# Optimization experiments

Measured on AMD Instinct MI355X. Metric: run time of the kernel, lower is better.

Reference implementation:

```python
import jax, jax.numpy as jnp
import numpy as np

B, U1, U2 = 4, 2048, 2048
C = 256      # in_feat_dim
F = 256      # feat_dim
M = 4        # num_modes
D = C // M   # attention_mode_dim = 64
ATTN_CLIP = 500.0
LN_EPS = 1e-12


def setup_inputs() -> dict:
    key = jax.random.key(0)
    ks = jax.random.split(key, 8)
    s = 0.02  # base_initializer_range
    inp = {
        "query_feat": jax.random.normal(ks[0], (B, U1, C), jnp.float32),
        "key_feat": jax.random.normal(ks[1], (B, U2, C), jnp.float32),
        "Wq": jax.random.normal(ks[2], (M * D, C), jnp.float32) * s,
        "bq": jnp.zeros((M * D,), jnp.float32),
    }
    # tie_qk_scheme='shared': key linear shares query weights
    inp["Wk"] = inp["Wq"]
    inp["bk"] = inp["bq"]
    inp["Wv"] = jax.random.normal(ks[3], (M * F, C), jnp.float32) * s  # first_linear, v_has_bias=False
    inp["W_mid"] = jax.random.normal(ks[4], (F, F), jnp.float32) * s   # MMSharedMid shared_linear
    inp["b_mid"] = jnp.zeros((F,), jnp.float32)
    inp["W_out"] = jax.random.normal(ks[5], (M, F, F), jnp.float32) * s  # grouped 1x1 conv, per mode
    inp["b_out"] = jnp.zeros((M, F), jnp.float32)
    inp["ln_g"] = jnp.ones((F,), jnp.float32)   # resout LayerNorm
    inp["ln_b"] = jnp.zeros((F,), jnp.float32)
    inp["W_score"] = jax.random.normal(ks[6], (1, F), jnp.float32) * s  # LearnedSoftAggregate
    inp["b_score"] = jnp.zeros((1,), jnp.float32)
    return inp


def _layer_norm(x, g, b):
    mu = jnp.mean(x, axis=-1, keepdims=True)
    var = jnp.var(x, axis=-1, keepdims=True)
    return (x - mu) * jax.lax.rsqrt(var + LN_EPS) * g + b


def reference(query_feat, key_feat, Wq, bq, Wk, bk, Wv, W_mid, b_mid,
              W_out, b_out, ln_g, ln_b, W_score, b_score):
    # --- tied-QK multi-mode attention ---
    q = (query_feat @ Wq.T + bq).reshape(B, U1, M, D)
    k = (key_feat @ Wk.T + bk).reshape(B, U2, M, D)
    scores = jnp.einsum('bimd,bjmd->bmij', q, k) / jnp.sqrt(jnp.float32(D))
    scores = jnp.clip(scores, -ATTN_CLIP, ATTN_CLIP)  # attn_clip
    probs = jax.nn.softmax(scores, axis=-1)           # [B, M, U1, U2]

    # --- ExpandedFeatTrans: value projection + fusion ---
    v = (key_feat @ Wv.T).reshape(B, U2, M, F)        # first_linear (no bias)
    fused = jnp.einsum('bmij,bjmf->bmif', probs, v)   # [B, M, U1, F]

    # MMSharedMid: shared linear over F + gelu (dropout = identity in eval)
    mid = jax.nn.gelu(fused @ W_mid.T + b_mid, approximate=False)

    # MMPrivateOutput: per-mode grouped 1x1 conv; NOTE the original code computes
    # x_comb = x + shortcut but then layer-norms x (shortcut dropped) - kept faithful.
    out = jnp.einsum('bmif,mgf->bmig', mid, W_out) + b_out[None, :, None, :]
    out = _layer_norm(out, ln_g, ln_b)                # [B, M, U1, F]

    # LearnedSoftAggregate over modes (group_dim=1, keepdim=False)
    mode_scores = out @ W_score.T + b_score           # [B, M, U1, 1]
    mode_probs = jax.nn.softmax(mode_scores, axis=1)
    return jnp.sum(out * mode_probs, axis=1)          # [B, U1, F]
```

## Files before the change

kernel.cpp:

```cpp
#include <hip/hip_runtime.h>

typedef __attribute__((ext_vector_type(8))) short short8;
typedef __attribute__((ext_vector_type(4))) float f32x4;
typedef __attribute__((ext_vector_type(16))) float f32x16;
typedef unsigned short u16t;
typedef unsigned int u32t;

#define MFMA16(a, b, c) __builtin_amdgcn_mfma_f32_16x16x32_bf16((a), (b), (c), 0, 0, 0)
#define MFMA32(a, b, c) __builtin_amdgcn_mfma_f32_32x32x16_bf16((a), (b), (c), 0, 0, 0)

__device__ __forceinline__ u16t f2bf(float f) {
  u32t u = __float_as_uint(f);
  u32t r = u + 0x7fffu + ((u >> 16) & 1u);
  return (u16t)(r >> 16);
}
__device__ __forceinline__ float bf2f(u16t b) {
  return __uint_as_float(((u32t)b) << 16);
}
__device__ __forceinline__ short8 pack8(float4 a0, float4 a1) {
  short8 r;
  r[0] = (short)f2bf(a0.x); r[1] = (short)f2bf(a0.y);
  r[2] = (short)f2bf(a0.z); r[3] = (short)f2bf(a0.w);
  r[4] = (short)f2bf(a1.x); r[5] = (short)f2bf(a1.y);
  r[6] = (short)f2bf(a1.z); r[7] = (short)f2bf(a1.w);
  return r;
}
__device__ __forceinline__ u32t packrhu(float a, float b) {
  u32t ua = __float_as_uint(a) + 0x8000u;
  u32t ub = __float_as_uint(b) + 0x8000u;
  return (ua >> 16) | (ub & 0xffff0000u);
}

__global__ __launch_bounds__(256) void prep_kernel(
    const float* __restrict__ query, const float* __restrict__ key,
    const float* __restrict__ Wq, const float* __restrict__ bq,
    const float* __restrict__ Wv, const float* __restrict__ Wm,
    const float* __restrict__ Wo,
    u16t* __restrict__ WmB, u16t* __restrict__ WoB,
    u16t* __restrict__ QfB, u16t* __restrict__ KfB, u16t* __restrict__ VfB) {
  const int blk = blockIdx.x;
  const int tid = threadIdx.x;

  if (blk >= 768) {
    int cv = blk - 768;
    const float* src; u16t* dst; int base;
    if (cv < 64) { src = Wm; dst = WmB; base = cv * 1024; }
    else         { src = Wo; dst = WoB; base = (cv - 64) * 1024; }
    int i = base + tid * 4;
    float4 v = *(const float4*)(src + i);
    ushort4 o2;
    o2.x = f2bf(v.x); o2.y = f2bf(v.y); o2.z = f2bf(v.z); o2.w = f2bf(v.w);
    *(ushort4*)(dst + i) = o2;
    return;
  }

  __shared__ __align__(16) u16t As[64 * 264];
  __shared__ __align__(16) u16t Ws[64 * 72];

  const int w = tid >> 6, lane = tid & 63, quad = lane >> 4, l15 = lane & 15;
  const int l31 = lane & 31, h8 = (lane >> 5) * 8;
  const int wrow = (w >> 1) * 32, wcol = (w & 1) * 32;
  const int r2 = tid >> 3, c8 = tid & 7;

  const float* A; const float* W; const float* bias;
  float scale; u16t* outp; int mode, bx, by0;
  if (blk < 128) {
    A = query; W = Wq; bias = bq; scale = 0.125f; outp = QfB; mode = 0; bx = blk; by0 = 0;
  } else if (blk < 256) {
    A = key; W = Wq; bias = bq; scale = 1.0f; outp = KfB; mode = 0; bx = blk - 128; by0 = 0;
  } else {
    int v2 = blk - 256;
    A = key; W = Wv; bias = nullptr; scale = 1.0f; outp = VfB; mode = 1;
    bx = v2 & 127; by0 = (v2 >> 7) * 4;
  }
  const int rt = bx * 64;

#pragma unroll
  for (int hh = 0; hh < 2; ++hh) {
    int rr = r2 + hh * 32;
    const float* arow = A + (size_t)(rt + rr) * 256;
#pragma unroll
    for (int kt = 0; kt < 4; ++kt) {
      const float4* pa = (const float4*)(arow + kt * 64 + c8 * 8);
      float4 a0 = pa[0], a1 = pa[1];
      a0.x *= scale; a0.y *= scale; a0.z *= scale; a0.w *= scale;
      a1.x *= scale; a1.y *= scale; a1.z *= scale; a1.w *= scale;
      *(short8*)&As[rr * 264 + kt * 64 + c8 * 8] = pack8(a0, a1);
    }
  }
  __syncthreads();

  short8 af[8][2];
#pragma unroll
  for (int ks8 = 0; ks8 < 8; ++ks8) {
    af[ks8][0] = *(const short8*)&As[(wrow + l15) * 264 + ks8 * 32 + quad * 8];
    af[ks8][1] = *(const short8*)&As[(wrow + 16 + l15) * 264 + ks8 * 32 + quad * 8];
  }

#pragma unroll 1
  for (int nt = 0; nt < 4; ++nt) {
    const int by = by0 + nt;
    const int ct = by * 64;

    const f32x4 fz = {0.f, 0.f, 0.f, 0.f};
    f32x4 acc[2][2];
#pragma unroll
    for (int i = 0; i < 2; i++)
#pragma unroll
      for (int j = 0; j < 2; j++) acc[i][j] = fz;

#pragma unroll
    for (int kt = 0; kt < 4; ++kt) {
      __syncthreads();
#pragma unroll
      for (int hh = 0; hh < 2; ++hh) {
        int rr = r2 + hh * 32;
        const float4* pw = (const float4*)(W + (size_t)(ct + rr) * 256 + kt * 64 + c8 * 8);
        *(short8*)&Ws[rr * 72 + c8 * 8] = pack8(pw[0], pw[1]);
      }
      __syncthreads();
#pragma unroll
      for (int ks = 0; ks < 2; ++ks) {
        short8 bw0 = *(const short8*)&Ws[(wcol + l15) * 72 + ks * 32 + quad * 8];
        short8 bw1 = *(const short8*)&Ws[(wcol + 16 + l15) * 72 + ks * 32 + quad * 8];
        acc[0][0] = MFMA16(af[kt * 2 + ks][0], bw0, acc[0][0]);
        acc[0][1] = MFMA16(af[kt * 2 + ks][0], bw1, acc[0][1]);
        acc[1][0] = MFMA16(af[kt * 2 + ks][1], bw0, acc[1][0]);
        acc[1][1] = MFMA16(af[kt * 2 + ks][1], bw1, acc[1][1]);
      }
    }

    __syncthreads();
    u16t* Cs = Ws;
    if (mode == 0) {
#pragma unroll
      for (int i = 0; i < 2; i++) {
        int rl = wrow + i * 16 + quad * 4;
#pragma unroll
        for (int j = 0; j < 2; j++) {
          int cl = wcol + j * 16 + l15;
          float bv = bias ? bias[ct + cl] * scale : 0.f;
#pragma unroll
          for (int rg = 0; rg < 4; ++rg)
            Cs[(rl + rg) * 72 + cl] = f2bf(acc[i][j][rg] + bv);
        }
      }
    } else {
#pragma unroll
      for (int i = 0; i < 2; i++) {
        int rl = wrow + i * 16 + quad * 4;
#pragma unroll
        for (int j = 0; j < 2; j++) {
          int cl = wcol + j * 16 + l15;
          ushort4 pk;
          pk.x = f2bf(acc[i][j][0]);
          pk.y = f2bf(acc[i][j][1]);
          pk.z = f2bf(acc[i][j][2]);
          pk.w = f2bf(acc[i][j][3]);
          *(ushort4*)&Cs[cl * 72 + rl] = pk;
        }
      }
    }
    __syncthreads();
#pragma unroll
    for (int t2 = 0; t2 < 2; ++t2) {
      short8 frag = *(const short8*)&Cs[(t2 * 32 + l31) * 72 + w * 16 + h8];
      size_t base;
      if (mode == 0) {
        int b = rt >> 11, m = by;
        int it32 = ((rt & 2047) >> 5) + t2;
        base = (((size_t)(b * 4 + m) * 64 + it32) * 4 + w) * 512;
      } else {
        int b = rt >> 11, m = by >> 2;
        int fb = ((by & 3) << 1) + t2;
        int jt16 = ((rt & 2047) >> 4) + w;
        base = (((size_t)(b * 4 + m) * 8 + fb) * 128 + jt16) * 512;
      }
      *(short8*)(outp + base + lane * 8) = frag;
    }
  }
}

__global__ __launch_bounds__(256, 4) void attn_kernel(
    const u16t* __restrict__ Qf, const u16t* __restrict__ Kf,
    const u16t* __restrict__ Vf,
    const u16t* __restrict__ Wmid, const u16t* __restrict__ Wout,
    const float* __restrict__ b_mid, const float* __restrict__ b_out,
    const float* __restrict__ ln_g, const float* __restrict__ ln_b,
    const float* __restrict__ Wsc, const float* __restrict__ b_sc,
    u16t* __restrict__ out_ln, float* __restrict__ scoresWS) {
  __shared__ __align__(16) u16t smU[8448];
  __shared__ float smL[128];
  __shared__ float smR[128];
  __shared__ float smS[64];
  const int tid = threadIdx.x;
  const int w = tid >> 6, lane = tid & 63, quad = lane >> 4, l15 = lane & 15;
  const int l31 = lane & 31, h = lane >> 5;
  const int L = blockIdx.x;
  const int xcd = L & 7, slot = L >> 3;
  const int bm = xcd * 2 + (slot >> 6);
  const int it32 = slot & 63;
  const int m = bm & 3;
  const int q0 = it32 * 32;

  const size_t lane8 = (size_t)lane * 8;

  const u16t* qbase = Qf + ((size_t)(bm * 64 + it32) * 4) * 512 + lane8;
  short8 qf4[4];
#pragma unroll
  for (int ksd = 0; ksd < 4; ++ksd)
    qf4[ksd] = *(const short8*)(qbase + ksd * 512);

  const u16t* kbase = Kf + ((size_t)bm * 256) * 512 + lane8;
  const u16t* vbase = Vf + ((size_t)(bm * 8 + 2 * w) * 128) * 512 + lane8;

  f32x16 facc[2];
#pragma unroll
  for (int j = 0; j < 2; j++)
#pragma unroll
    for (int r = 0; r < 16; r++) facc[j][r] = 0.f;
  float lsum = 0.f;

  short8 kf4[4];
#pragma unroll
  for (int ksd = 0; ksd < 4; ++ksd)
    kf4[ksd] = *(const short8*)(kbase + (size_t)w * 2048 + ksd * 512);

  {
    f32x16 sacc;
#pragma unroll
    for (int r = 0; r < 16; r++) sacc[r] = 0.f;
#pragma unroll
    for (int ksd = 0; ksd < 4; ++ksd)
      sacc = MFMA32(kf4[ksd], qf4[ksd], sacc);
    float ls = 0.f;
#pragma unroll
    for (int tt = 0; tt < 8; ++tt) {
      const int jl = ((2 * tt) & 3) + 8 * ((2 * tt) >> 2) + 4 * h;
      float p0 = __expf(sacc[2 * tt]);
      float p1 = __expf(sacc[2 * tt + 1]);
      ls += p0 + p1;
      *(u32t*)&smU[l31 * 132 + w * 32 + jl] = packrhu(p0, p1);
    }
    lsum += ls;
  }
#pragma unroll
  for (int ksd = 0; ksd < 4; ++ksd)
    kf4[ksd] = *(const short8*)(kbase + (size_t)(4 + w) * 2048 + ksd * 512);
  __syncthreads();

#pragma unroll 1
  for (int t = 0; t < 16; ++t) {
    u16t* Pb = (t & 1) ? smU + 4224 : smU;
    u16t* Pn = (t & 1) ? smU : smU + 4224;

    if (t < 15) {
      f32x16 sacc;
#pragma unroll
      for (int r = 0; r < 16; r++) sacc[r] = 0.f;
#pragma unroll
      for (int ksd = 0; ksd < 4; ++ksd)
        sacc = MFMA32(kf4[ksd], qf4[ksd], sacc);
      float ls = 0.f;
#pragma unroll
      for (int tt = 0; tt < 8; ++tt) {
        const int jl = ((2 * tt) & 3) + 8 * ((2 * tt) >> 2) + 4 * h;
        float p0 = __expf(sacc[2 * tt]);
        float p1 = __expf(sacc[2 * tt + 1]);
        ls += p0 + p1;
        *(u32t*)&Pn[l31 * 132 + w * 32 + jl] = packrhu(p0, p1);
      }
      lsum += ls;
    }
    if (t < 14) {
      const int jn = (t + 2) * 4 + w;
#pragma unroll
      for (int ksd = 0; ksd < 4; ++ksd)
        kf4[ksd] = *(const short8*)(kbase + (size_t)jn * 2048 + ksd * 512);
    }
#pragma unroll
    for (int jj = 0; jj < 4; ++jj) {
      short8 vf[2][2];
#pragma unroll
      for (int fb = 0; fb < 2; ++fb)
#pragma unroll
        for (int ks2 = 0; ks2 < 2; ++ks2)
          vf[fb][ks2] = *(const short8*)(vbase + ((size_t)fb * 128 + (t * 8 + jj * 2 + ks2)) * 512);
      short8 bbL[2];
#pragma unroll
      for (int ks2 = 0; ks2 < 2; ++ks2)
        bbL[ks2] = *(const short8*)&Pb[l31 * 132 + jj * 32 + ks2 * 16 + h * 8];
      facc[0] = MFMA32(vf[0][0], bbL[0], facc[0]);
      facc[0] = MFMA32(vf[0][1], bbL[1], facc[0]);
      facc[1] = MFMA32(vf[1][0], bbL[0], facc[1]);
      facc[1] = MFMA32(vf[1][1], bbL[1], facc[1]);
    }
    __syncthreads();
  }

  lsum += __shfl_xor(lsum, 32);
  if (h == 0) smL[w * 32 + l31] = lsum;
  __syncthreads();
  float inv = 1.f / (smL[l31] + smL[32 + l31] + smL[64 + l31] + smL[96 + l31]);

  u16t* const smF = smU;
#pragma unroll
  for (int fb = 0; fb < 2; ++fb) {
#pragma unroll
    for (int g = 0; g < 4; ++g) {
      int fbase = w * 64 + fb * 32 + 8 * g + 4 * h;
      ushort4 pk4;
      pk4.x = f2bf(facc[fb][4 * g + 0] * inv);
      pk4.y = f2bf(facc[fb][4 * g + 1] * inv);
      pk4.z = f2bf(facc[fb][4 * g + 2] * inv);
      pk4.w = f2bf(facc[fb][4 * g + 3] * inv);
      *(ushort4*)&smF[l31 * 264 + fbase] = pk4;
    }
  }
  __syncthreads();

  const int rgrp = w >> 1, ch = w & 1;
  const int rowq = rgrp * 16 + quad * 4;
  const f32x4 fz4 = {0.f, 0.f, 0.f, 0.f};

  f32x4 macc[8];
#pragma unroll
  for (int i = 0; i < 8; i++) macc[i] = fz4;
  for (int kc = 0; kc < 8; ++kc) {
    short8 af = *(const short8*)&smF[(rgrp * 16 + l15) * 264 + kc * 32 + quad * 8];
#pragma unroll
    for (int nb = 0; nb < 8; ++nb) {
      short8 bw = *(const short8*)(Wmid + (size_t)(ch * 128 + nb * 16 + l15) * 256 + kc * 32 + quad * 8);
      macc[nb] = MFMA16(af, bw, macc[nb]);
    }
  }
#pragma unroll
  for (int nb = 0; nb < 8; ++nb) {
    int c = ch * 128 + nb * 16 + l15;
    float bmv = b_mid[c];
#pragma unroll
    for (int rg = 0; rg < 4; ++rg) {
      float x = macc[nb][rg] + bmv;
      macc[nb][rg] = 0.5f * x * (1.f + erff(x * 0.70710678118654752f));
    }
  }
  __syncthreads();
#pragma unroll
  for (int nb = 0; nb < 8; ++nb)
#pragma unroll
    for (int rg = 0; rg < 4; ++rg)
      smF[(rowq + rg) * 264 + ch * 128 + nb * 16 + l15] = f2bf(macc[nb][rg]);
  __syncthreads();

  const u16t* Wo = Wout + (size_t)m * 65536;
  f32x4 oacc[8];
#pragma unroll
  for (int i = 0; i < 8; i++) oacc[i] = fz4;
  for (int kc = 0; kc < 8; ++kc) {
    short8 af = *(const short8*)&smF[(rgrp * 16 + l15) * 264 + kc * 32 + quad * 8];
#pragma unroll
    for (int nb = 0; nb < 8; ++nb) {
      short8 bw = *(const short8*)(Wo + (size_t)(ch * 128 + nb * 16 + l15) * 256 + kc * 32 + quad * 8);
      oacc[nb] = MFMA16(af, bw, oacc[nb]);
    }
  }

  float sum[4] = {0, 0, 0, 0}, sq[4] = {0, 0, 0, 0};
#pragma unroll
  for (int nb = 0; nb < 8; ++nb) {
    int c = ch * 128 + nb * 16 + l15;
    float bo = b_out[m * 256 + c];
#pragma unroll
    for (int rg = 0; rg < 4; ++rg) {
      float x = oacc[nb][rg] + bo;
      oacc[nb][rg] = x;
      sum[rg] += x;
      sq[rg] += x * x;
    }
  }
#pragma unroll
  for (int rg = 0; rg < 4; ++rg) {
    float s = sum[rg], s2 = sq[rg];
    s += __shfl_xor(s, 1); s += __shfl_xor(s, 2); s += __shfl_xor(s, 4); s += __shfl_xor(s, 8);
    s2 += __shfl_xor(s2, 1); s2 += __shfl_xor(s2, 2); s2 += __shfl_xor(s2, 4); s2 += __shfl_xor(s2, 8);
    if (l15 == 0) {
      smR[(rowq + rg) + 32 * ch] = s;
      smR[64 + (rowq + rg) + 32 * ch] = s2;
    }
  }
  __syncthreads();
  float mu[4], rstd[4];
#pragma unroll
  for (int rg = 0; rg < 4; ++rg) {
    int r = rowq + rg;
    float s = smR[r] + smR[r + 32];
    float s2 = smR[64 + r] + smR[64 + r + 32];
    float mean = s * (1.f / 256.f);
    float var = s2 * (1.f / 256.f) - mean * mean;
    mu[rg] = mean;
    rstd[rg] = rsqrtf(var + 1e-12f);
  }

  float scp[4] = {0, 0, 0, 0};
#pragma unroll
  for (int nb = 0; nb < 8; ++nb) {
    int c = ch * 128 + nb * 16 + l15;
    float g = ln_g[c], bb2 = ln_b[c], wsv = Wsc[c];
#pragma unroll
    for (int rg = 0; rg < 4; ++rg) {
      float xn = (oacc[nb][rg] - mu[rg]) * rstd[rg] * g + bb2;
      out_ln[((size_t)bm * 2048 + (q0 + rowq + rg)) * 256 + c] = f2bf(xn);
      scp[rg] += xn * wsv;
    }
  }
#pragma unroll
  for (int rg = 0; rg < 4; ++rg) {
    float s = scp[rg];
    s += __shfl_xor(s, 1); s += __shfl_xor(s, 2); s += __shfl_xor(s, 4); s += __shfl_xor(s, 8);
    if (l15 == 0) smS[(rowq + rg) + 32 * ch] = s;
  }
  __syncthreads();
  if (ch == 0 && l15 == 0) {
#pragma unroll
    for (int rg = 0; rg < 4; ++rg) {
      int r = rowq + rg;
      scoresWS[bm * 2048 + q0 + r] = smS[r] + smS[r + 32] + b_sc[0];
    }
  }
}

__global__ __launch_bounds__(256) void agg_kernel(
    const u16t* __restrict__ out_ln, const float* __restrict__ scoresWS,
    float* __restrict__ out) {
  const int row = blockIdx.x;
  const int c = threadIdx.x;
  const int b = row >> 11, i = row & 2047;
  float s0 = scoresWS[(b * 4 + 0) * 2048 + i];
  float s1 = scoresWS[(b * 4 + 1) * 2048 + i];
  float s2 = scoresWS[(b * 4 + 2) * 2048 + i];
  float s3 = scoresWS[(b * 4 + 3) * 2048 + i];
  float mx = fmaxf(fmaxf(s0, s1), fmaxf(s2, s3));
  float e0 = __expf(s0 - mx), e1 = __expf(s1 - mx), e2 = __expf(s2 - mx), e3 = __expf(s3 - mx);
  float inv = 1.f / (e0 + e1 + e2 + e3);
  float acc = e0 * inv * bf2f(out_ln[((size_t)(b * 4 + 0) * 2048 + i) * 256 + c]) +
              e1 * inv * bf2f(out_ln[((size_t)(b * 4 + 1) * 2048 + i) * 256 + c]) +
              e2 * inv * bf2f(out_ln[((size_t)(b * 4 + 2) * 2048 + i) * 256 + c]) +
              e3 * inv * bf2f(out_ln[((size_t)(b * 4 + 3) * 2048 + i) * 256 + c]);
  out[(size_t)row * 256 + c] = acc;
}

extern "C" void kernel_launch(void* const* d_in, const int* in_sizes, int n_in,
                              void* d_out, int out_size, void* d_ws, size_t ws_size,
                              hipStream_t stream) {
  (void)in_sizes; (void)n_in; (void)out_size; (void)ws_size;
  const float* query = (const float*)d_in[0];
  const float* key   = (const float*)d_in[1];
  const float* Wq    = (const float*)d_in[2];
  const float* bq    = (const float*)d_in[3];
  const float* Wv    = (const float*)d_in[6];
  const float* Wm    = (const float*)d_in[7];
  const float* bmid  = (const float*)d_in[8];
  const float* Wo    = (const float*)d_in[9];
  const float* bo    = (const float*)d_in[10];
  const float* lng   = (const float*)d_in[11];
  const float* lnb   = (const float*)d_in[12];
  const float* Wsc   = (const float*)d_in[13];
  const float* bsc   = (const float*)d_in[14];

  char* p = (char*)d_ws;
  u16t* QfB = (u16t*)p; p += (size_t)2097152 * 2;
  u16t* KfB = (u16t*)p; p += (size_t)2097152 * 2;
  u16t* VfB = (u16t*)p; p += (size_t)8388608 * 2;
  u16t* WmB = (u16t*)p; p += (size_t)65536 * 2;
  u16t* WoB = (u16t*)p; p += (size_t)262144 * 2;
  u16t* outLn = (u16t*)p; p += (size_t)8388608 * 2;
  float* scWS = (float*)p; p += (size_t)32768 * 4;

  prep_kernel<<<1088, 256, 0, stream>>>(query, key, Wq, bq, Wv, Wm, Wo,
                                        WmB, WoB, QfB, KfB, VfB);

  attn_kernel<<<1024, 256, 0, stream>>>(QfB, KfB, VfB, WmB, WoB,
                                        bmid, bo, lng, lnb, Wsc, bsc,
                                        outLn, scWS);

  agg_kernel<<<8192, 256, 0, stream>>>(outLn, scWS, (float*)d_out);
}
```

Measured before the change: 236.7 us.

## Keep softmax probabilities in registers via cross-lane shuffles, removing LDS staging and barriers

Before, the four waves split the key tiles, wrote exp-scores to double-buffered shared memory and synchronised with block barriers before the PV MFMA. Now each wave computes the scores for every key tile itself and rearranges the packed bf16 probabilities into the B-operand layout with __shfl_xor across lane halves. The per-iteration LDS round trip, the block barriers and the cross-wave row-sum reduction go away. In exchange each wave performs all 64 QK MFMA tiles and exponentials instead of a quarter of them, so QK compute and K loads grow by four times.

```diff
diff --git a/kernel.cpp b/kernel.cpp
--- a/kernel.cpp
+++ b/kernel.cpp
@@ -3,6 +3,7 @@
 typedef __attribute__((ext_vector_type(8))) short short8;
 typedef __attribute__((ext_vector_type(4))) float f32x4;
 typedef __attribute__((ext_vector_type(16))) float f32x16;
+typedef __attribute__((ext_vector_type(4))) unsigned int u32x4;
 typedef unsigned short u16t;
 typedef unsigned int u32t;
 
@@ -189,8 +190,7 @@
     const float* __restrict__ ln_g, const float* __restrict__ ln_b,
     const float* __restrict__ Wsc, const float* __restrict__ b_sc,
     u16t* __restrict__ out_ln, float* __restrict__ scoresWS) {
-  __shared__ __align__(16) u16t smU[8448];
-  __shared__ float smL[128];
+  __shared__ __align__(16) u16t smF[8448];
   __shared__ float smR[128];
   __shared__ float smS[64];
   const int tid = threadIdx.x;
@@ -224,86 +224,62 @@
   short8 kf4[4];
 #pragma unroll
   for (int ksd = 0; ksd < 4; ++ksd)
-    kf4[ksd] = *(const short8*)(kbase + (size_t)w * 2048 + ksd * 512);
-
-  {
+    kf4[ksd] = *(const short8*)(kbase + ksd * 512);
+
+#pragma unroll 1
+  for (int jt = 0; jt < 64; ++jt) {
     f32x16 sacc;
 #pragma unroll
     for (int r = 0; r < 16; r++) sacc[r] = 0.f;
 #pragma unroll
     for (int ksd = 0; ksd < 4; ++ksd)
       sacc = MFMA32(kf4[ksd], qf4[ksd], sacc);
+
+    if (jt < 63) {
+#pragma unroll
+      for (int ksd = 0; ksd < 4; ++ksd)
+        kf4[ksd] = *(const short8*)(kbase + (size_t)(jt + 1) * 2048 + ksd * 512);
+    }
+
+    short8 vf00 = *(const short8*)(vbase + ((size_t)(2 * jt)) * 512);
+    short8 vf01 = *(const short8*)(vbase + ((size_t)(2 * jt + 1)) * 512);
+    short8 vf10 = *(const short8*)(vbase + ((size_t)(128 + 2 * jt)) * 512);
+    short8 vf11 = *(const short8*)(vbase + ((size_t)(128 + 2 * jt + 1)) * 512);
+
+    float ev[16];
+#pragma unroll
+    for (int r = 0; r < 16; ++r) ev[r] = __expf(sacc[r]);
     float ls = 0.f;
 #pragma unroll
-    for (int tt = 0; tt < 8; ++tt) {
-      const int jl = ((2 * tt) & 3) + 8 * ((2 * tt) >> 2) + 4 * h;
-      float p0 = __expf(sacc[2 * tt]);
-      float p1 = __expf(sacc[2 * tt + 1]);
-      ls += p0 + p1;
-      *(u32t*)&smU[l31 * 132 + w * 32 + jl] = packrhu(p0, p1);
-    }
+    for (int r = 0; r < 16; ++r) ls += ev[r];
     lsum += ls;
-  }
-#pragma unroll
-  for (int ksd = 0; ksd < 4; ++ksd)
-    kf4[ksd] = *(const short8*)(kbase + (size_t)(4 + w) * 2048 + ksd * 512);
-  __syncthreads();
-
-#pragma unroll 1
-  for (int t = 0; t < 16; ++t) {
-    u16t* Pb = (t & 1) ? smU + 4224 : smU;
-    u16t* Pn = (t & 1) ? smU : smU + 4224;
-
-    if (t < 15) {
-      f32x16 sacc;
-#pragma unroll
-      for (int r = 0; r < 16; r++) sacc[r] = 0.f;
-#pragma unroll
-      for (int ksd = 0; ksd < 4; ++ksd)
-        sacc = MFMA32(kf4[ksd], qf4[ksd], sacc);
-      float ls = 0.f;
-#pragma unroll
-      for (int tt = 0; tt < 8; ++tt) {
-        const int jl = ((2 * tt) & 3) + 8 * ((2 * tt) >> 2) + 4 * h;
-        float p0 = __expf(sacc[2 * tt]);
-        float p1 = __expf(sacc[2 * tt + 1]);
-        ls += p0 + p1;
-        *(u32t*)&Pn[l31 * 132 + w * 32 + jl] = packrhu(p0, p1);
-      }
-      lsum += ls;
-    }
-    if (t < 14) {
-      const int jn = (t + 2) * 4 + w;
-#pragma unroll
-      for (int ksd = 0; ksd < 4; ++ksd)
-        kf4[ksd] = *(const short8*)(kbase + (size_t)jn * 2048 + ksd * 512);
-    }
-#pragma unroll
-    for (int jj = 0; jj < 4; ++jj) {
-      short8 vf[2][2];
-#pragma unroll
-      for (int fb = 0; fb < 2; ++fb)
-#pragma unroll
-        for (int ks2 = 0; ks2 < 2; ++ks2)
-          vf[fb][ks2] = *(const short8*)(vbase + ((size_t)fb * 128 + (t * 8 + jj * 2 + ks2)) * 512);
-      short8 bbL[2];
-#pragma unroll
-      for (int ks2 = 0; ks2 < 2; ++ks2)
-        bbL[ks2] = *(const short8*)&Pb[l31 * 132 + jj * 32 + ks2 * 16 + h * 8];
-      facc[0] = MFMA32(vf[0][0], bbL[0], facc[0]);
-      facc[0] = MFMA32(vf[0][1], bbL[1], facc[0]);
-      facc[1] = MFMA32(vf[1][0], bbL[0], facc[1]);
-      facc[1] = MFMA32(vf[1][1], bbL[1], facc[1]);
-    }
-    __syncthreads();
+    u32t pk[8];
+#pragma unroll
+    for (int t2 = 0; t2 < 8; ++t2) pk[t2] = packrhu(ev[2 * t2], ev[2 * t2 + 1]);
+    u32t sx[8];
+#pragma unroll
+    for (int t2 = 0; t2 < 8; ++t2) sx[t2] = __shfl_xor(pk[t2], 32);
+    u32x4 F0, F1;
+    F0[0] = h ? sx[2] : pk[0];
+    F0[1] = h ? sx[3] : pk[1];
+    F0[2] = h ? pk[2] : sx[0];
+    F0[3] = h ? pk[3] : sx[1];
+    F1[0] = h ? sx[6] : pk[4];
+    F1[1] = h ? sx[7] : pk[5];
+    F1[2] = h ? pk[6] : sx[4];
+    F1[3] = h ? pk[7] : sx[5];
+    short8 frag0 = *(short8*)&F0;
+    short8 frag1 = *(short8*)&F1;
+
+    facc[0] = MFMA32(vf00, frag0, facc[0]);
+    facc[0] = MFMA32(vf01, frag1, facc[0]);
+    facc[1] = MFMA32(vf10, frag0, facc[1]);
+    facc[1] = MFMA32(vf11, frag1, facc[1]);
   }
 
   lsum += __shfl_xor(lsum, 32);
-  if (h == 0) smL[w * 32 + l31] = lsum;
-  __syncthreads();
-  float inv = 1.f / (smL[l31] + smL[32 + l31] + smL[64 + l31] + smL[96 + l31]);
-
-  u16t* const smF = smU;
+  float inv = 1.f / lsum;
+
 #pragma unroll
   for (int fb = 0; fb < 2; ++fb) {
 #pragma unroll
```

Result: slower. 255.1 us (+7.8%).

## Pre-convert projection weights to bf16 and double-buffer weight tiles in projection GEMM

Applied to the files above, without the earlier changes.

Splits the prep kernel into a weight-conversion kernel (Wq, Wv, Wm, Wo to bf16) and a projection kernel that reads bf16 weights directly. The projection loop now double-buffers the weight tile in shared memory, prefetching the next k-slice into registers while computing, which cuts one barrier per step and halves weight load bytes. It adds an extra kernel launch and serialises conversion before projection, and the output staging now reuses the A tile buffer.

```diff
diff --git a/kernel.cpp b/kernel.cpp
--- a/kernel.cpp
+++ b/kernel.cpp
@@ -31,46 +31,48 @@
   return (ua >> 16) | (ub & 0xffff0000u);
 }
 
-__global__ __launch_bounds__(256) void prep_kernel(
+__global__ __launch_bounds__(256) void cvt_kernel(
+    const float* __restrict__ Wq, const float* __restrict__ Wv,
+    const float* __restrict__ Wm, const float* __restrict__ Wo,
+    u16t* __restrict__ WqB, u16t* __restrict__ WvB,
+    u16t* __restrict__ WmB, u16t* __restrict__ WoB) {
+  const int blk = blockIdx.x, tid = threadIdx.x;
+  const float* src; u16t* dst; int base;
+  if (blk < 64)       { src = Wq; dst = WqB; base = blk * 1024; }
+  else if (blk < 320) { src = Wv; dst = WvB; base = (blk - 64) * 1024; }
+  else if (blk < 384) { src = Wm; dst = WmB; base = (blk - 320) * 1024; }
+  else                { src = Wo; dst = WoB; base = (blk - 384) * 1024; }
+  int i = base + tid * 4;
+  float4 v = *(const float4*)(src + i);
+  ushort4 o;
+  o.x = f2bf(v.x); o.y = f2bf(v.y); o.z = f2bf(v.z); o.w = f2bf(v.w);
+  *(ushort4*)(dst + i) = o;
+}
+
+__global__ __launch_bounds__(256) void proj_kernel(
     const float* __restrict__ query, const float* __restrict__ key,
-    const float* __restrict__ Wq, const float* __restrict__ bq,
-    const float* __restrict__ Wv, const float* __restrict__ Wm,
-    const float* __restrict__ Wo,
-    u16t* __restrict__ WmB, u16t* __restrict__ WoB,
+    const u16t* __restrict__ WqB, const u16t* __restrict__ WvB,
+    const float* __restrict__ bq,
     u16t* __restrict__ QfB, u16t* __restrict__ KfB, u16t* __restrict__ VfB) {
+  __shared__ __align__(16) u16t As[64 * 264];
+  __shared__ __align__(16) u16t Ws[2][64 * 72];
+
   const int blk = blockIdx.x;
   const int tid = threadIdx.x;
-
-  if (blk >= 768) {
-    int cv = blk - 768;
-    const float* src; u16t* dst; int base;
-    if (cv < 64) { src = Wm; dst = WmB; base = cv * 1024; }
-    else         { src = Wo; dst = WoB; base = (cv - 64) * 1024; }
-    int i = base + tid * 4;
-    float4 v = *(const float4*)(src + i);
-    ushort4 o2;
-    o2.x = f2bf(v.x); o2.y = f2bf(v.y); o2.z = f2bf(v.z); o2.w = f2bf(v.w);
-    *(ushort4*)(dst + i) = o2;
-    return;
-  }
-
-  __shared__ __align__(16) u16t As[64 * 264];
-  __shared__ __align__(16) u16t Ws[64 * 72];
-
   const int w = tid >> 6, lane = tid & 63, quad = lane >> 4, l15 = lane & 15;
   const int l31 = lane & 31, h8 = (lane >> 5) * 8;
   const int wrow = (w >> 1) * 32, wcol = (w & 1) * 32;
   const int r2 = tid >> 3, c8 = tid & 7;
 
-  const float* A; const float* W; const float* bias;
+  const float* A; const u16t* W16; const float* bias;
   float scale; u16t* outp; int mode, bx, by0;
   if (blk < 128) {
-    A = query; W = Wq; bias = bq; scale = 0.125f; outp = QfB; mode = 0; bx = blk; by0 = 0;
+    A = query; W16 = WqB; bias = bq; scale = 0.125f; outp = QfB; mode = 0; bx = blk; by0 = 0;
   } else if (blk < 256) {
-    A = key; W = Wq; bias = bq; scale = 1.0f; outp = KfB; mode = 0; bx = blk - 128; by0 = 0;
+    A = key; W16 = WqB; bias = bq; scale = 1.0f; outp = KfB; mode = 0; bx = blk - 128; by0 = 0;
   } else {
     int v2 = blk - 256;
-    A = key; W = Wv; bias = nullptr; scale = 1.0f; outp = VfB; mode = 1;
+    A = key; W16 = WvB; bias = nullptr; scale = 1.0f; outp = VfB; mode = 1;
     bx = v2 & 127; by0 = (v2 >> 7) * 4;
   }
   const int rt = bx * 64;
@@ -97,41 +99,60 @@
     af[ks8][1] = *(const short8*)&As[(wrow + 16 + l15) * 264 + ks8 * 32 + quad * 8];
   }
 
+#pragma unroll
+  for (int hh = 0; hh < 2; ++hh) {
+    int rr = r2 + hh * 32;
+    *(short8*)&Ws[0][rr * 72 + c8 * 8] =
+        *(const short8*)(W16 + (size_t)(by0 * 64 + rr) * 256 + c8 * 8);
+  }
+  __syncthreads();
+
+  const f32x4 fz = {0.f, 0.f, 0.f, 0.f};
+  f32x4 acc[2][2];
+#pragma unroll
+  for (int i = 0; i < 2; i++)
+#pragma unroll
+    for (int j = 0; j < 2; j++) acc[i][j] = fz;
+
 #pragma unroll 1
   for (int nt = 0; nt < 4; ++nt) {
     const int by = by0 + nt;
     const int ct = by * 64;
 
-    const f32x4 fz = {0.f, 0.f, 0.f, 0.f};
-    f32x4 acc[2][2];
-#pragma unroll
-    for (int i = 0; i < 2; i++)
-#pragma unroll
-      for (int j = 0; j < 2; j++) acc[i][j] = fz;
-
 #pragma unroll
     for (int kt = 0; kt < 4; ++kt) {
-      __syncthreads();
-#pragma unroll
-      for (int hh = 0; hh < 2; ++hh) {
-        int rr = r2 + hh * 32;
-        const float4* pw = (const float4*)(W + (size_t)(ct + rr) * 256 + kt * 64 + c8 * 8);
-        *(short8*)&Ws[rr * 72 + c8 * 8] = pack8(pw[0], pw[1]);
-      }
-      __syncthreads();
+      short8 wst[2];
+      const bool havenext = (nt < 3) || (kt < 3);
+      if (havenext) {
+        const int ctn = (kt < 3) ? ct : (ct + 64);
+        const int ktn = (kt + 1) & 3;
+#pragma unroll
+        for (int hh = 0; hh < 2; ++hh) {
+          int rr = r2 + hh * 32;
+          wst[hh] = *(const short8*)(W16 + (size_t)(ctn + rr) * 256 + ktn * 64 + c8 * 8);
+        }
+      }
+      const u16t* Wb = &Ws[kt & 1][0];
 #pragma unroll
       for (int ks = 0; ks < 2; ++ks) {
-        short8 bw0 = *(const short8*)&Ws[(wcol + l15) * 72 + ks * 32 + quad * 8];
-        short8 bw1 = *(const short8*)&Ws[(wcol + 16 + l15) * 72 + ks * 32 + quad * 8];
+        short8 bw0 = *(const short8*)&Wb[(wcol + l15) * 72 + ks * 32 + quad * 8];
+        short8 bw1 = *(const short8*)&Wb[(wcol + 16 + l15) * 72 + ks * 32 + quad * 8];
         acc[0][0] = MFMA16(af[kt * 2 + ks][0], bw0, acc[0][0]);
         acc[0][1] = MFMA16(af[kt * 2 + ks][0], bw1, acc[0][1]);
         acc[1][0] = MFMA16(af[kt * 2 + ks][1], bw0, acc[1][0]);
         acc[1][1] = MFMA16(af[kt * 2 + ks][1], bw1, acc[1][1]);
       }
-    }
-
-    __syncthreads();
-    u16t* Cs = Ws;
+      if (havenext) {
+#pragma unroll
+        for (int hh = 0; hh < 2; ++hh) {
+          int rr = r2 + hh * 32;
+          *(short8*)&Ws[(kt + 1) & 1][rr * 72 + c8 * 8] = wst[hh];
+        }
+      }
+      __syncthreads();
+    }
+
+    u16t* Cs = As;
     if (mode == 0) {
 #pragma unroll
       for (int i = 0; i < 2; i++) {
@@ -178,6 +199,10 @@
       }
       *(short8*)(outp + base + lane * 8) = frag;
     }
+#pragma unroll
+    for (int i = 0; i < 2; i++)
+#pragma unroll
+      for (int j = 0; j < 2; j++) acc[i][j] = fz;
   }
 }
 
@@ -473,11 +498,15 @@
   u16t* VfB = (u16t*)p; p += (size_t)8388608 * 2;
   u16t* WmB = (u16t*)p; p += (size_t)65536 * 2;
   u16t* WoB = (u16t*)p; p += (size_t)262144 * 2;
+  u16t* WqB = (u16t*)p; p += (size_t)65536 * 2;
+  u16t* WvB = (u16t*)p; p += (size_t)262144 * 2;
   u16t* outLn = (u16t*)p; p += (size_t)8388608 * 2;
   float* scWS = (float*)p; p += (size_t)32768 * 4;
 
-  prep_kernel<<<1088, 256, 0, stream>>>(query, key, Wq, bq, Wv, Wm, Wo,
-                                        WmB, WoB, QfB, KfB, VfB);
+  cvt_kernel<<<640, 256, 0, stream>>>(Wq, Wv, Wm, Wo, WqB, WvB, WmB, WoB);
+
+  proj_kernel<<<768, 256, 0, stream>>>(query, key, WqB, WvB, bq,
+                                       QfB, KfB, VfB);
 
   attn_kernel<<<1024, 256, 0, stream>>>(QfB, KfB, VfB, WmB, WoB,
                                         bmid, bo, lng, lnb, Wsc, bsc,
```

Result: no change. 235.0 us (median of 2 runs) (-0.8%).
